# Kernel optimization log

Measured on AMD Instinct MI355X. Metric: run time of the kernel, lower is better.

Reference implementation:

```python
import jax, jax.numpy as jnp
import numpy as np

N_NODES = 40000

def setup_inputs() -> dict:
    key = jax.random.key(0)
    k1, k2, k3, k4 = jax.random.split(key, 4)
    x = jax.random.normal(k1, (N_NODES, 256), dtype=jnp.float32)
    edge_index = jax.random.randint(k2, (2, 640000), 0, N_NODES, dtype=jnp.int64)
    W = jax.random.normal(k3, (256, 128), dtype=jnp.float32) * (1.0 / np.sqrt(256))
    b = jax.random.normal(k4, (128,), dtype=jnp.float32) * 0.01
    return {"x": x, "edge_index": edge_index, "W": W, "b": b}

def reference(x, edge_index, W, b):
    N = x.shape[0]
    # GCNConv: add self-loops, symmetric degree normalization, linear, aggregate, bias
    loops = jnp.arange(N, dtype=edge_index.dtype)
    src = jnp.concatenate([edge_index[0], loops])  # message sources j
    dst = jnp.concatenate([edge_index[1], loops])  # targets i
    ones = jnp.ones_like(dst, dtype=x.dtype)
    deg = jax.ops.segment_sum(ones, dst, num_segments=N)  # in-degree incl. self-loop
    dinv = jnp.where(deg > 0, jax.lax.rsqrt(deg), 0.0)
    norm = dinv[src] * dinv[dst]  # [E+N]
    xw = x @ W  # transform first (in_dim -> out_dim), as in PyG GCNConv
    msgs = norm[:, None] * xw[src]  # [E+N, out_dim]
    agg = jax.ops.segment_sum(msgs, dst, num_segments=N) + b
    return jax.nn.relu(agg)  # dropout_value == 0 -> no dropout
```

## Files before the change

kernel.cpp:

```cpp
#include <hip/hip_runtime.h>

#define N_NODES 40000
#define IN_DIM 256
#define OUT_DIM 128
#define CAP 64
#define GEMM_BLOCKS 625
#define FILL_BLOCKS 625

typedef __bf16 bf16x8 __attribute__((ext_vector_type(8)));
typedef float floatx4 __attribute__((ext_vector_type(4)));

__device__ __forceinline__ int clamp_idx(int v) {
    unsigned u = (unsigned)v;
    return (u < (unsigned)N_NODES) ? v : 0;
}

__device__ __forceinline__ int get_idx(const void* p, long long i, int is64) {
    if (is64) return clamp_idx((int)((const long long*)p)[i]);
    return clamp_idx(((const int*)p)[i]);
}

__device__ __forceinline__ float bflo(unsigned u) {
    union { unsigned i; float f; } c; c.i = u << 16; return c.f;
}
__device__ __forceinline__ float bfhi(unsigned u) {
    union { unsigned i; float f; } c; c.i = u & 0xFFFF0000u; return c.f;
}

__global__ void prep_r12(const int* __restrict__ edge32, int* __restrict__ flag,
                         int* __restrict__ cnt, const float* __restrict__ W,
                         __bf16* __restrict__ wswz) {
    int i = blockIdx.x * 256 + threadIdx.x;
    if (i < N_NODES) cnt[i] = 0;
    if (i < IN_DIM * OUT_DIM) {
        int j    = i & 7;
        int lane = (i >> 3) & 63;
        int tile = i >> 9;
        int ct = tile & 7, kc = tile >> 3;
        int k = kc * 32 + (lane >> 4) * 8 + j;
        int n = ct * 16 + (lane & 15);
        wswz[i] = (__bf16)W[k * OUT_DIM + n];
    }
    if (blockIdx.x == 0) {
        __shared__ int sh[256];
        int t = threadIdx.x;
        int nz = 0;
        for (int k = t; k < 1000; k += 256) nz |= (edge32[2 * k + 1] != 0);
        sh[t] = nz;
        __syncthreads();
        for (int off = 128; off > 0; off >>= 1) {
            if (t < off) sh[t] |= sh[t + off];
            __syncthreads();
        }
        if (t == 0) *flag = sh[0] ? 0 : 1;
    }
}

__global__ __launch_bounds__(256) void main_r12(
    const float* __restrict__ x, const __bf16* __restrict__ wswz,
    __bf16* __restrict__ xwb,
    const void* __restrict__ edge, int E, const int* __restrict__ flag,
    int* __restrict__ cnt, unsigned short* __restrict__ bucket) {
    int t = threadIdx.x;
    if (blockIdx.x < GEMM_BLOCKS) {
        int wave = t >> 6, lane = t & 63;
        int quad = lane >> 4, m16 = lane & 15;
        int m = blockIdx.x * 64 + wave * 16 + m16;
        const float* xrow = x + (long long)m * IN_DIM;
        const bf16x8* wp = (const bf16x8*)wswz;

        floatx4 acc[8];
#pragma unroll
        for (int ct = 0; ct < 8; ++ct) acc[ct] = (floatx4){0.f, 0.f, 0.f, 0.f};

#pragma unroll
        for (int kc = 0; kc < 8; ++kc) {
            int k0 = kc * 32 + quad * 8;
            float4 xa = *(const float4*)(xrow + k0);
            float4 xb = *(const float4*)(xrow + k0 + 4);
            bf16x8 af;
            af[0] = (__bf16)xa.x; af[1] = (__bf16)xa.y;
            af[2] = (__bf16)xa.z; af[3] = (__bf16)xa.w;
            af[4] = (__bf16)xb.x; af[5] = (__bf16)xb.y;
            af[6] = (__bf16)xb.z; af[7] = (__bf16)xb.w;
#pragma unroll
            for (int ct = 0; ct < 8; ++ct) {
                bf16x8 bf = wp[(kc * 8 + ct) * 64 + lane];
                acc[ct] = __builtin_amdgcn_mfma_f32_16x16x32_bf16(af, bf, acc[ct], 0, 0, 0);
            }
        }

        int rbase = blockIdx.x * 64 + wave * 16 + quad * 4;
#pragma unroll
        for (int ct = 0; ct < 8; ++ct) {
            int col = ct * 16 + m16;
#pragma unroll
            for (int r = 0; r < 4; ++r)
                xwb[(long long)(rbase + r) * OUT_DIM + col] = (__bf16)acc[ct][r];
        }
    } else {
        int is64 = *flag;
        int base = (blockIdx.x - GEMM_BLOCKS) * 1024 + t * 4;
        int s0 = get_idx(edge, base + 0, is64);
        int s1 = get_idx(edge, base + 1, is64);
        int s2 = get_idx(edge, base + 2, is64);
        int s3 = get_idx(edge, base + 3, is64);
        int d0 = get_idx(edge, (long long)E + base + 0, is64);
        int d1 = get_idx(edge, (long long)E + base + 1, is64);
        int d2 = get_idx(edge, (long long)E + base + 2, is64);
        int d3 = get_idx(edge, (long long)E + base + 3, is64);
        int p0 = atomicAdd(&cnt[d0], 1);
        int p1 = atomicAdd(&cnt[d1], 1);
        int p2 = atomicAdd(&cnt[d2], 1);
        int p3 = atomicAdd(&cnt[d3], 1);
        if (p0 < CAP) bucket[d0 * CAP + p0] = (unsigned short)s0;
        if (p1 < CAP) bucket[d1 * CAP + p1] = (unsigned short)s1;
        if (p2 < CAP) bucket[d2 * CAP + p2] = (unsigned short)s2;
        if (p3 < CAP) bucket[d3 * CAP + p3] = (unsigned short)s3;
    }
}

__global__ void gather_r12(const unsigned short* __restrict__ bucket,
                           const int* __restrict__ cnt,
                           const unsigned* __restrict__ xwd, const float* __restrict__ b,
                           float* __restrict__ out) {
    int node = blockIdx.x * 4 + (threadIdx.x >> 6);
    int lane = threadIdx.x & 63;
    if (node >= N_NODES) return;
    float b0 = b[2 * lane], b1 = b[2 * lane + 1];
    int cn_true = cnt[node];
    int take = cn_true < CAP ? cn_true : CAP;
    float dd = rsqrtf((float)(cn_true + 1));
    unsigned us = xwd[node * 64 + lane];
    float a0 = dd * dd * bflo(us);
    float a1 = dd * dd * bfhi(us);

    int s_l = 0; float nrm_l = 0.0f;
    if (lane < take) {
        s_l = (int)bucket[node * CAP + lane];
        nrm_l = dd * rsqrtf((float)(cnt[s_l] + 1));
    }
    int j = 0;
    for (; j + 8 <= take; j += 8) {
        int   s0 = __shfl(s_l, j),     s1 = __shfl(s_l, j + 1);
        int   s2 = __shfl(s_l, j + 2), s3 = __shfl(s_l, j + 3);
        int   s4 = __shfl(s_l, j + 4), s5 = __shfl(s_l, j + 5);
        int   s6 = __shfl(s_l, j + 6), s7 = __shfl(s_l, j + 7);
        float n0 = __shfl(nrm_l, j),     n1 = __shfl(nrm_l, j + 1);
        float n2 = __shfl(nrm_l, j + 2), n3 = __shfl(nrm_l, j + 3);
        float n4 = __shfl(nrm_l, j + 4), n5 = __shfl(nrm_l, j + 5);
        float n6 = __shfl(nrm_l, j + 6), n7 = __shfl(nrm_l, j + 7);
        unsigned u0 = xwd[s0 * 64 + lane], u1 = xwd[s1 * 64 + lane];
        unsigned u2 = xwd[s2 * 64 + lane], u3 = xwd[s3 * 64 + lane];
        unsigned u4 = xwd[s4 * 64 + lane], u5 = xwd[s5 * 64 + lane];
        unsigned u6 = xwd[s6 * 64 + lane], u7 = xwd[s7 * 64 + lane];
        a0 += n0 * bflo(u0); a1 += n0 * bfhi(u0);
        a0 += n1 * bflo(u1); a1 += n1 * bfhi(u1);
        a0 += n2 * bflo(u2); a1 += n2 * bfhi(u2);
        a0 += n3 * bflo(u3); a1 += n3 * bfhi(u3);
        a0 += n4 * bflo(u4); a1 += n4 * bfhi(u4);
        a0 += n5 * bflo(u5); a1 += n5 * bfhi(u5);
        a0 += n6 * bflo(u6); a1 += n6 * bfhi(u6);
        a0 += n7 * bflo(u7); a1 += n7 * bfhi(u7);
    }
    for (; j < take; ++j) {
        int   s = __shfl(s_l, j);
        float n = __shfl(nrm_l, j);
        unsigned u = xwd[s * 64 + lane];
        a0 += n * bflo(u); a1 += n * bfhi(u);
    }
    float2 r;
    r.x = fmaxf(a0 + b0, 0.0f);
    r.y = fmaxf(a1 + b1, 0.0f);
    *(float2*)&out[node * OUT_DIM + 2 * lane] = r;
}

extern "C" void kernel_launch(void* const* d_in, const int* in_sizes, int n_in,
                              void* d_out, int out_size, void* d_ws, size_t ws_size,
                              hipStream_t stream) {
    const float* x   = (const float*)d_in[0];
    const void* edge = d_in[1];
    const float* W   = (const float*)d_in[2];
    const float* b   = (const float*)d_in[3];
    float* out       = (float*)d_out;

    int E = in_sizes[1] / 2;

    char* ws = (char*)d_ws;
    int*            cnt    = (int*)(ws);
    int*            flag   = (int*)(ws + 160000);
    __bf16*         wswz   = (__bf16*)(ws + 160256);
    unsigned short* bucket = (unsigned short*)(ws + 225792);
    __bf16*         xwb    = (__bf16*)(ws + 5345792);

    prep_r12<<<160, 256, 0, stream>>>((const int*)edge, flag, cnt, W, wswz);
    main_r12<<<GEMM_BLOCKS + FILL_BLOCKS, 256, 0, stream>>>(
        x, wswz, xwb, edge, E, flag, cnt, bucket);
    gather_r12<<<N_NODES / 4, 256, 0, stream>>>(bucket, cnt, (const unsigned*)xwb, b, out);
}
```

Baseline: 152.3 us.

## Partition bucket fill by destination range so each block writes a local node range

The edge-bucket fill now splits edges into 160 slices and destination nodes into 8 ranges. Each fill block scans one slice and handles only the edges whose destination falls in its range. Atomics and bucket writes per block should then hit a contiguous node range, and, if consecutive blocks land on different XCDs, each XCD's L2 sees a localized part of cnt/bucket. The cost is that every edge's destination index is read 8 times, the fill block count rises from 625 to 1280, and `blockIdx.x & 7` is used as the range, which assumes GEMM_BLOCKS alignment and still covers all ranges.

```diff
diff --git a/kernel.cpp b/kernel.cpp
--- a/kernel.cpp
+++ b/kernel.cpp
@@ -5,7 +5,10 @@
 #define OUT_DIM 128
 #define CAP 64
 #define GEMM_BLOCKS 625
-#define FILL_BLOCKS 625
+#define FILL_SLICES 160
+#define FILL_RANGES 8
+#define FILL_BLOCKS (FILL_SLICES * FILL_RANGES)
+#define RANGE_SZ ((N_NODES + FILL_RANGES - 1) / FILL_RANGES)
 
 typedef __bf16 bf16x8 __attribute__((ext_vector_type(8)));
 typedef float floatx4 __attribute__((ext_vector_type(4)));
@@ -27,7 +30,7 @@
     union { unsigned i; float f; } c; c.i = u & 0xFFFF0000u; return c.f;
 }
 
-__global__ void prep_r12(const int* __restrict__ edge32, int* __restrict__ flag,
+__global__ void prep_r13(const int* __restrict__ edge32, int* __restrict__ flag,
                          int* __restrict__ cnt, const float* __restrict__ W,
                          __bf16* __restrict__ wswz) {
     int i = blockIdx.x * 256 + threadIdx.x;
@@ -56,7 +59,7 @@
     }
 }
 
-__global__ __launch_bounds__(256) void main_r12(
+__global__ __launch_bounds__(256) void main_r13(
     const float* __restrict__ x, const __bf16* __restrict__ wswz,
     __bf16* __restrict__ xwb,
     const void* __restrict__ edge, int E, const int* __restrict__ flag,
@@ -100,27 +103,25 @@
         }
     } else {
         int is64 = *flag;
-        int base = (blockIdx.x - GEMM_BLOCKS) * 1024 + t * 4;
-        int s0 = get_idx(edge, base + 0, is64);
-        int s1 = get_idx(edge, base + 1, is64);
-        int s2 = get_idx(edge, base + 2, is64);
-        int s3 = get_idx(edge, base + 3, is64);
-        int d0 = get_idx(edge, (long long)E + base + 0, is64);
-        int d1 = get_idx(edge, (long long)E + base + 1, is64);
-        int d2 = get_idx(edge, (long long)E + base + 2, is64);
-        int d3 = get_idx(edge, (long long)E + base + 3, is64);
-        int p0 = atomicAdd(&cnt[d0], 1);
-        int p1 = atomicAdd(&cnt[d1], 1);
-        int p2 = atomicAdd(&cnt[d2], 1);
-        int p3 = atomicAdd(&cnt[d3], 1);
-        if (p0 < CAP) bucket[d0 * CAP + p0] = (unsigned short)s0;
-        if (p1 < CAP) bucket[d1 * CAP + p1] = (unsigned short)s1;
-        if (p2 < CAP) bucket[d2 * CAP + p2] = (unsigned short)s2;
-        if (p3 < CAP) bucket[d3 * CAP + p3] = (unsigned short)s3;
-    }
-}
-
-__global__ void gather_r12(const unsigned short* __restrict__ bucket,
+        int fb = blockIdx.x - GEMM_BLOCKS;
+        int range = blockIdx.x & 7;
+        int slice = fb >> 3;
+        int lo = range * RANGE_SZ;
+        int slice_len = (E + FILL_SLICES - 1) / FILL_SLICES;
+        int e0 = slice * slice_len;
+        int e1 = e0 + slice_len; if (e1 > E) e1 = E;
+        for (int e = e0 + t; e < e1; e += 256) {
+            int d = get_idx(edge, (long long)E + e, is64);
+            if ((unsigned)(d - lo) < (unsigned)RANGE_SZ) {
+                int s = get_idx(edge, e, is64);
+                int pos = atomicAdd(&cnt[d], 1);
+                if (pos < CAP) bucket[d * CAP + pos] = (unsigned short)s;
+            }
+        }
+    }
+}
+
+__global__ void gather_r13(const unsigned short* __restrict__ bucket,
                            const int* __restrict__ cnt,
                            const unsigned* __restrict__ xwd, const float* __restrict__ b,
                            float* __restrict__ out) {
@@ -193,8 +194,8 @@
     unsigned short* bucket = (unsigned short*)(ws + 225792);
     __bf16*         xwb    = (__bf16*)(ws + 5345792);
 
-    prep_r12<<<160, 256, 0, stream>>>((const int*)edge, flag, cnt, W, wswz);
-    main_r12<<<GEMM_BLOCKS + FILL_BLOCKS, 256, 0, stream>>>(
+    prep_r13<<<160, 256, 0, stream>>>((const int*)edge, flag, cnt, W, wswz);
+    main_r13<<<GEMM_BLOCKS + FILL_BLOCKS, 256, 0, stream>>>(
         x, wswz, xwb, edge, E, flag, cnt, bucket);
-    gather_r12<<<N_NODES / 4, 256, 0, stream>>>(bucket, cnt, (const unsigned*)xwb, b, out);
-}
+    gather_r13<<<N_NODES / 4, 256, 0, stream>>>(bucket, cnt, (const unsigned*)xwb, b, out);
+}
```

Result: slower. 157.7 us (+3.6%).
